# Performance work log

Hardware: AMD Instinct MI355X
Metric: run time of the kernel (lower is better)

## Reference

```python
import jax, jax.numpy as jnp
import numpy as np
from jax import lax

B_SZ = 64
D_MODEL = 768
D_INNER = 1536   # expand * d_model
D_STATE = 16
D_CONV = 4
DT_RANK = 48     # ceil(768/16)
ROWS, COLS = 16, 16
L = ROWS * COLS
LN_EPS = 1e-5


def setup_inputs() -> dict:
    key = jax.random.key(0)
    ks = jax.random.split(key, 16)
    def nrm(k, shape, s):
        return jax.random.normal(k, shape, jnp.float32) * s
    # A_log init as in Mamba: log(arange(1..d_state)) tiled over d_inner
    A_log = jnp.log(jnp.tile(jnp.arange(1, D_STATE + 1, dtype=jnp.float32)[None, :], (D_INNER, 1)))
    # dt bias init: inverse-softplus of dt ~ LogUniform(1e-3, 1e-1)
    def dt_bias_init(k):
        u = jax.random.uniform(k, (D_INNER,), jnp.float32)
        dt = jnp.exp(u * (np.log(0.1) - np.log(0.001)) + np.log(0.001))
        return dt + jnp.log(-jnp.expm1(-dt))
    dt_std = DT_RANK ** -0.5
    return {
        "hidden_states": jax.random.normal(ks[0], (B_SZ, L, D_MODEL), jnp.float32),
        "in_proj_w": nrm(ks[1], (2 * D_INNER, D_MODEL), 0.02),
        "conv_w": nrm(ks[2], (D_INNER, D_CONV), 0.2),
        "conv_bias": nrm(ks[3], (D_INNER,), 0.1),
        "conv_w_b": nrm(ks[4], (D_INNER, D_CONV), 0.2),
        "conv_bias_b": nrm(ks[5], (D_INNER,), 0.1),
        "x_proj_w": nrm(ks[6], (DT_RANK + 2 * D_STATE, D_INNER), 0.02),
        "x_proj_w_b": nrm(ks[7], (DT_RANK + 2 * D_STATE, D_INNER), 0.02),
        "dt_proj_w": jax.random.uniform(ks[8], (D_INNER, DT_RANK), jnp.float32, -dt_std, dt_std),
        "dt_proj_w_b": jax.random.uniform(ks[9], (D_INNER, DT_RANK), jnp.float32, -dt_std, dt_std),
        "dt_bias": dt_bias_init(ks[10]),
        "dt_bias_b": dt_bias_init(ks[11]),
        "A_log": A_log,
        "A_b_log": A_log,
        "Dp": jnp.ones((D_INNER,), jnp.float32),
        "Dp_b": jnp.ones((D_INNER,), jnp.float32),
        "ln_gamma": jnp.ones((D_INNER,), jnp.float32),
        "ln_beta": jnp.zeros((D_INNER,), jnp.float32),
        "out_proj_w": nrm(ks[12], (D_MODEL, D_INNER), 0.02),
    }


def _causal_conv_silu(x, w, b):
    # x: (B, D, L); depthwise causal conv (left-pad K-1) + SiLU
    y = lax.conv_general_dilated(x, w[:, None, :], (1,), [(D_CONV - 1, 0)],
                                 dimension_numbers=("NCH", "OIH", "NCH"),
                                 feature_group_count=D_INNER)
    return jax.nn.silu(y + b[None, :, None])


def _selective_scan(u, dt, A_log, Bm, Cm, dt_bias):
    # u, dt: (B, D, Lr); Bm, Cm: (B, N, Lr)
    A = -jnp.exp(A_log)                                     # (D, N)
    delta = jax.nn.softplus(dt + dt_bias[None, :, None])    # (B, D, Lr)
    dA = jnp.exp(jnp.einsum("bdl,dn->lbdn", delta, A))     # (Lr, B, D, N)
    dBu = jnp.einsum("bdl,bnl,bdl->lbdn", delta, Bm, u)    # (Lr, B, D, N)
    C_l = jnp.moveaxis(Cm, -1, 0)                           # (Lr, B, N)
    def step(h, inp):
        dA_t, dBu_t, C_t = inp
        h = dA_t * h + dBu_t
        return h, jnp.einsum("bdn,bn->bd", h, C_t)
    h0 = jnp.zeros(dA.shape[1:], dA.dtype)
    _, ys = lax.scan(step, h0, (dA, dBu, C_l))
    return jnp.moveaxis(ys, 0, -1)                          # (B, D, Lr)


def _direction(x, conv_w, conv_bias, x_proj_w, dt_proj_w, dt_bias, A_log, Dp):
    xc = _causal_conv_silu(x, conv_w, conv_bias)            # (B, D, L)
    x_comp = xc.reshape(-1, D_INNER, ROWS, COLS).mean(axis=3)  # (B, D, ROWS)
    x_dbl = jnp.einsum("bdl,ed->ble", x_comp, x_proj_w)    # (B, ROWS, R+2N)
    dt, Bm, Cm = jnp.split(x_dbl, [DT_RANK, DT_RANK + D_STATE], axis=-1)
    dt = jnp.einsum("blr,dr->bdl", dt, dt_proj_w)          # (B, D, ROWS)
    Bm = jnp.moveaxis(Bm, 1, 2)                             # (B, N, ROWS)
    Cm = jnp.moveaxis(Cm, 1, 2)
    y = _selective_scan(x_comp, dt, A_log, Bm, Cm, dt_bias)
    return jnp.repeat(y, COLS, axis=2) + Dp[None, :, None] * xc  # (B, D, L)


def reference(hidden_states, in_proj_w, conv_w, conv_bias, conv_w_b, conv_bias_b,
              x_proj_w, x_proj_w_b, dt_proj_w, dt_proj_w_b, dt_bias, dt_bias_b,
              A_log, A_b_log, Dp, Dp_b, ln_gamma, ln_beta, out_proj_w):
    xz = jnp.einsum("bld,ed->bel", hidden_states, in_proj_w)  # (B, 2*Di, L)
    x, z = jnp.split(xz, 2, axis=1)
    out_f = _direction(x, conv_w, conv_bias, x_proj_w, dt_proj_w, dt_bias, A_log, Dp)
    out_b = _direction(x[:, :, ::-1], conv_w_b, conv_bias_b, x_proj_w_b, dt_proj_w_b, dt_bias_b, A_b_log, Dp_b)
    comb = jnp.moveaxis((out_f + out_b[:, :, ::-1]) * 0.5, 1, 2)  # (B, L, Di)
    mu = comb.mean(-1, keepdims=True)
    var = comb.var(-1, keepdims=True)
    normed = (comb - mu) * lax.rsqrt(var + LN_EPS) * ln_gamma + ln_beta
    gated = normed * jax.nn.silu(jnp.moveaxis(z, 1, 2))
    return jnp.einsum("bld,od->blo", gated, out_proj_w)       # (B, L, d_model)
```

## Files before the change

kernel.cpp:

```cpp
#include <hip/hip_runtime.h>
#include <cstdint>
#include <cstddef>

typedef __bf16 bf16_t;
typedef __attribute__((ext_vector_type(2))) __bf16 bf16x2;
typedef __attribute__((ext_vector_type(8))) __bf16 bf16x8;
typedef __attribute__((ext_vector_type(4))) float f32x4;
typedef __attribute__((ext_vector_type(2))) float f32x2;

#define NB     64
#define LSEQ   256
#define DM     768
#define DI     1536
#define NSTATE 16
#define NROWS  16
#define RANK   48

#define BF16_PROBE 0x3F803F80u

__device__ __forceinline__ float bf2f(bf16_t v) { return (float)v; }

__device__ __forceinline__ float ldp(const void* p, size_t i, bool isbf) {
  return isbf ? (float)((const bf16_t*)p)[i] : ((const float*)p)[i];
}

__device__ __forceinline__ float silu_f(float x) {
  const float e = __expf(-fabsf(x));
  return (x >= 0.f) ? (x / (1.f + e)) : (x * e / (1.f + e));
}

__device__ __forceinline__ void async16(const bf16_t* g, bf16_t* l) {
  __builtin_amdgcn_global_load_lds(
      (const __attribute__((address_space(1))) void*)g,
      (__attribute__((address_space(3))) void*)l, 16, 0, 0);
}

__device__ __forceinline__ void cvt8(const void* in, bf16_t* out, int i, bool isbf) {
  if (isbf) {
    ((bf16x8*)out)[i] = ((const bf16x8*)in)[i];
  } else {
    const float* f = (const float*)in + (size_t)i * 8;
    f32x4 lo = *(const f32x4*)f, hi = *(const f32x4*)(f + 4);
    ((bf16x8*)out)[i] = (bf16x8){(bf16_t)lo.x, (bf16_t)lo.y, (bf16_t)lo.z, (bf16_t)lo.w,
                                 (bf16_t)hi.x, (bf16_t)hi.y, (bf16_t)hi.z, (bf16_t)hi.w};
  }
}

#define PREP_NH    6144
#define PREP_NWIN  1152
#define PREP_NWOUT 576
__global__ __launch_bounds__(256) void prep_kernel(
    const void* __restrict__ H, const void* __restrict__ Win,
    const void* __restrict__ Wout,
    bf16_t* __restrict__ Hb, bf16_t* __restrict__ Winb, bf16_t* __restrict__ Woutb,
    const uint32_t* __restrict__ probe)
{
  const bool isbf = (probe[0] == BF16_PROBE);
  int blk = blockIdx.x;
  if (blk < PREP_NH) {
    cvt8(H, Hb, blk * 256 + threadIdx.x, isbf);
  } else if (blk < PREP_NH + PREP_NWIN) {
    cvt8(Win, Winb, (blk - PREP_NH) * 256 + threadIdx.x, isbf);
  } else {
    cvt8(Wout, Woutb, (blk - PREP_NH - PREP_NWIN) * 256 + threadIdx.x, isbf);
  }
}

#define LDS_IDX(ab, db, half) (((ab) << 2) + ((db) << 1) + (half))

#define STAGE(ab, db, half, kt) do {                                          \
    const int _kt = ((kt) < NT) ? (kt) : (NT - 1);                            \
    const bf16_t* _g = (ab) ? B : A;                                          \
    const size_t _rb = ((ab) ? bn : bm) + (size_t)((half) * 128);             \
    bf16_t* _l = &sm[LDS_IDX(ab, db, half)][0];                               \
    _Pragma("unroll")                                                         \
    for (int _j = 0; _j < 2; _j++) {                                          \
      const int _c = wave * 2 + _j;                                           \
      async16(_g + (_rb + _c * 8 + srow) * (size_t)K + (size_t)_kt * 64 + scol,\
              _l + _c * 512);                                                 \
    }                                                                         \
  } while (0)

#define LOAD_A(db, mg) do {                                                   \
    _Pragma("unroll")                                                         \
    for (int _t = 0; _t < 2; _t++) {                                          \
      const int _mt = (mg) * 2 + _t;                                          \
      const int _lr = _mt * 32 + wm * 16 + r;                                 \
      const bf16_t* _b = &sm[LDS_IDX(0, db, _mt >> 2)][(_lr & 127) * 64];     \
      _Pragma("unroll")                                                       \
      for (int _s = 0; _s < 2; _s++)                                          \
        af[_t][_s] = *(const bf16x8*)&_b[(((_s * 4 + quad) ^ r7) * 8)];       \
    }                                                                         \
  } while (0)

#define LOAD_B(db) do {                                                       \
    _Pragma("unroll")                                                         \
    for (int _nt = 0; _nt < 4; _nt++) {                                       \
      const int _lr = _nt * 64 + wn * 16 + r;                                 \
      const bf16_t* _b = &sm[LDS_IDX(1, db, _lr >> 7)][(_lr & 127) * 64];     \
      _Pragma("unroll")                                                       \
      for (int _s = 0; _s < 2; _s++)                                          \
        bfr[_nt][_s] = *(const bf16x8*)&_b[(((_s * 4 + quad) ^ r7) * 8)];     \
    }                                                                         \
  } while (0)

#define MFMA16(mg) do {                                                       \
    __builtin_amdgcn_s_setprio(1);                                            \
    _Pragma("unroll")                                                         \
    for (int _t = 0; _t < 2; _t++)                                            \
    _Pragma("unroll")                                                         \
    for (int _nt = 0; _nt < 4; _nt++)                                         \
    _Pragma("unroll")                                                         \
    for (int _s = 0; _s < 2; _s++)                                            \
      acc[(mg) * 2 + _t][_nt] = __builtin_amdgcn_mfma_f32_16x16x32_bf16(      \
          af[_t][_s], bfr[_nt][_s], acc[(mg) * 2 + _t][_nt], 0, 0, 0);        \
    __builtin_amdgcn_s_setprio(0);                                            \
  } while (0)

#define BAR()    __builtin_amdgcn_s_barrier()
#define WAITL0() asm volatile("s_waitcnt lgkmcnt(0)" ::: "memory")
#define WAITV6() asm volatile("s_waitcnt vmcnt(6)" ::: "memory")

__global__ __launch_bounds__(512, 2) void gemm256_kernel(
    const bf16_t* __restrict__ A, const bf16_t* __restrict__ B,
    void* __restrict__ C, int M, int N, int K, int mode,
    bf16_t* __restrict__ xb)
{
  __shared__ bf16_t sm[8][8192];
  const int tid  = threadIdx.x;
  const int wave = tid >> 6, lane = tid & 63;
  const int wm = wave >> 2, wn = wave & 3;
  const int r = lane & 15, quad = lane >> 4, r7 = lane & 7;
  const int srow = lane >> 3;
  const int scol = ((lane & 7) ^ srow) * 8;
  const int NT = K >> 6;

  const int nwg  = gridDim.x * gridDim.y;
  const int orig = blockIdx.y * gridDim.x + blockIdx.x;
  const int swz  = (orig & 7) * (nwg >> 3) + (orig >> 3);
  const size_t bm = (size_t)(swz / gridDim.x) * 256;
  const size_t bn = (size_t)(swz % gridDim.x) * 256;

  f32x4 acc[8][4];
#pragma unroll
  for (int i = 0; i < 8; i++)
#pragma unroll
    for (int j = 0; j < 4; j++) acc[i][j] = (f32x4){0.f, 0.f, 0.f, 0.f};

  bf16x8 af[2][2];
  bf16x8 bfr[4][2];

  STAGE(1, 0, 0, 0);  STAGE(1, 0, 1, 0);  STAGE(0, 0, 0, 0);  STAGE(0, 0, 1, 0);
  asm volatile("s_waitcnt vmcnt(4)" ::: "memory");
  STAGE(1, 1, 0, 1);  STAGE(1, 1, 1, 1);  STAGE(0, 1, 0, 1);
  WAITV6();
  BAR();

  const int NP = NT >> 1;
  for (int i = 0; i < NP; ++i) {
    const int t1 = 2 * i + 1, t2 = 2 * i + 2, t3 = 2 * i + 3;
    LOAD_B(0); LOAD_A(0, 0); STAGE(0, 1, 1, t1);
    BAR(); WAITL0(); MFMA16(0); BAR();

    LOAD_A(0, 1); STAGE(1, 0, 0, t2);
    BAR(); WAITL0(); MFMA16(1); BAR();

    LOAD_A(0, 2); STAGE(1, 0, 1, t2);
    BAR(); WAITL0(); MFMA16(2); BAR();

    LOAD_A(0, 3); STAGE(0, 0, 0, t2);
    WAITV6();
    BAR(); WAITL0(); MFMA16(3); BAR();

    LOAD_B(1); LOAD_A(1, 0); STAGE(0, 0, 1, t2);
    BAR(); WAITL0(); MFMA16(0); BAR();

    LOAD_A(1, 1); STAGE(1, 1, 0, t3);
    BAR(); WAITL0(); MFMA16(1); BAR();

    LOAD_A(1, 2); STAGE(1, 1, 1, t3);
    BAR(); WAITL0(); MFMA16(2); BAR();

    LOAD_A(1, 3); STAGE(0, 1, 0, t3);
    WAITV6();
    BAR(); WAITL0(); MFMA16(3); BAR();
  }

  const int col16 = lane & 15;
  const int rb4 = quad * 4;

  if (mode == 0) {
#pragma unroll
    for (int mt = 0; mt < 8; mt++)
#pragma unroll
      for (int nt = 0; nt < 4; nt++)
#pragma unroll
        for (int v = 0; v < 4; v++) {
          const size_t m = bm + mt * 32 + wm * 16 + rb4 + v;
          const size_t n = bn + nt * 64 + wn * 16 + col16;
          ((float*)C)[m * (size_t)N + n] = acc[mt][nt][v];
        }
  } else {
    bf16_t* dst = (bn < (size_t)DI) ? xb : (bf16_t*)C;
    const size_t cb0 = (bn < (size_t)DI) ? bn : bn - DI;
#pragma unroll
    for (int mt = 0; mt < 8; mt++)
#pragma unroll
      for (int nt = 0; nt < 4; nt++)
#pragma unroll
        for (int v = 0; v < 4; v++) {
          const size_t m = bm + mt * 32 + wm * 16 + rb4 + v;
          dst[m * DI + cb0 + nt * 64 + wn * 16 + col16] = (bf16_t)acc[mt][nt][v];
        }
  }
}

__global__ __launch_bounds__(256) void conv_kernel(
    const bf16_t* __restrict__ xb,
    const void* __restrict__ cw_f, const void* __restrict__ cb_f,
    const void* __restrict__ cw_b, const void* __restrict__ cb_b,
    bf16_t* __restrict__ xc_f, bf16_t* __restrict__ xc_b,
    float* __restrict__ comp_f, float* __restrict__ comp_b,
    const uint32_t* __restrict__ probe)
{
  const bool isbf = (probe[0] == BF16_PROBE);
  int bi = blockIdx.x;
  const int chunk = bi & 3;
  bi >>= 2;
  const int b = bi / 3;
  const int pblk = bi % 3;
  const int d0 = (pblk * 256 + threadIdx.x) * 2;
  const int lr0 = chunk * 64;

  const float wf0a = ldp(cw_f, (size_t)d0 * 4 + 0, isbf),
              wf1a = ldp(cw_f, (size_t)d0 * 4 + 1, isbf),
              wf2a = ldp(cw_f, (size_t)d0 * 4 + 2, isbf),
              wf3a = ldp(cw_f, (size_t)d0 * 4 + 3, isbf);
  const float wf0c = ldp(cw_f, (size_t)(d0 + 1) * 4 + 0, isbf),
              wf1c = ldp(cw_f, (size_t)(d0 + 1) * 4 + 1, isbf),
              wf2c = ldp(cw_f, (size_t)(d0 + 1) * 4 + 2, isbf),
              wf3c = ldp(cw_f, (size_t)(d0 + 1) * 4 + 3, isbf);
  const float wb0a = ldp(cw_b, (size_t)d0 * 4 + 0, isbf),
              wb1a = ldp(cw_b, (size_t)d0 * 4 + 1, isbf),
              wb2a = ldp(cw_b, (size_t)d0 * 4 + 2, isbf),
              wb3a = ldp(cw_b, (size_t)d0 * 4 + 3, isbf);
  const float wb0c = ldp(cw_b, (size_t)(d0 + 1) * 4 + 0, isbf),
              wb1c = ldp(cw_b, (size_t)(d0 + 1) * 4 + 1, isbf),
              wb2c = ldp(cw_b, (size_t)(d0 + 1) * 4 + 2, isbf),
              wb3c = ldp(cw_b, (size_t)(d0 + 1) * 4 + 3, isbf);
  const float bfa = ldp(cb_f, d0, isbf), bfc = ldp(cb_f, d0 + 1, isbf);
  const float bba = ldp(cb_b, d0, isbf), bbc = ldp(cb_b, d0 + 1, isbf);

  const bf16_t* xrow = xb + (size_t)b * LSEQ * DI + d0;

  float t0a = 0.f, t1a = 0.f, t2a = 0.f, t3a = 0.f;
  float t0c = 0.f, t1c = 0.f, t2c = 0.f, t3c = 0.f;
  if (lr0 > 0) {
    bf16x2 v;
    v = *(const bf16x2*)&xrow[(size_t)(lr0 - 3) * DI]; t1a = (float)v.x; t1c = (float)v.y;
    v = *(const bf16x2*)&xrow[(size_t)(lr0 - 2) * DI]; t2a = (float)v.x; t2c = (float)v.y;
    v = *(const bf16x2*)&xrow[(size_t)(lr0 - 1) * DI]; t3a = (float)v.x; t3c = (float)v.y;
  }

  float sfa = 0.f, sfc = 0.f;
  float sba = 0.f, sbc = 0.f;
  for (int l = lr0; l < lr0 + 67; ++l) {
    float xa = 0.f, xcv = 0.f;
    if (l < LSEQ) {
      bf16x2 v = *(const bf16x2*)&xrow[(size_t)l * DI];
      xa = (float)v.x; xcv = (float)v.y;
    }
    t0a = t1a; t1a = t2a; t2a = t3a; t3a = xa;
    t0c = t1c; t1c = t2c; t2c = t3c; t3c = xcv;

    if (l < lr0 + 64) {
      const float ya = silu_f(bfa + wf0a * t0a + wf1a * t1a + wf2a * t2a + wf3a * t3a);
      const float yc = silu_f(bfc + wf0c * t0c + wf1c * t1c + wf2c * t2c + wf3c * t3c);
      *(bf16x2*)&xc_f[((size_t)b * LSEQ + l) * DI + d0] = (bf16x2){(bf16_t)ya, (bf16_t)yc};
      sfa += ya; sfc += yc;
      if ((l & 15) == 15) {
        *(f32x2*)&comp_f[((size_t)b * NROWS + (l >> 4)) * DI + d0] =
            (f32x2){sfa * (1.f / 16.f), sfc * (1.f / 16.f)};
        sfa = 0.f; sfc = 0.f;
      }
    }
    if (l >= lr0 + 3) {
      const int j = 258 - l;
      const float ya = silu_f(bba + wb0a * t3a + wb1a * t2a + wb2a * t1a + wb3a * t0a);
      const float yc = silu_f(bbc + wb0c * t3c + wb1c * t2c + wb2c * t1c + wb3c * t0c);
      *(bf16x2*)&xc_b[((size_t)b * LSEQ + j) * DI + d0] = (bf16x2){(bf16_t)ya, (bf16_t)yc};
      sba += ya; sbc += yc;
      if ((j & 15) == 0) {
        *(f32x2*)&comp_b[((size_t)b * NROWS + (j >> 4)) * DI + d0] =
            (f32x2){sba * (1.f / 16.f), sbc * (1.f / 16.f)};
        sba = 0.f; sbc = 0.f;
      }
    }
  }
}

__global__ __launch_bounds__(256) void xproj_kernel(
    const float* __restrict__ comp_f, const float* __restrict__ comp_b,
    const void* __restrict__ w_f, const void* __restrict__ w_b,
    float* __restrict__ xd_f, float* __restrict__ xd_b,
    const uint32_t* __restrict__ probe)
{
  const bool isbf = (probe[0] == BF16_PROBE);
  const int dir = blockIdx.y;
  const int rg = blockIdx.x;
  const float* comp = dir ? comp_b : comp_f;
  const void* W = dir ? w_b : w_f;
  float* out = dir ? xd_b : xd_f;
  const int r0 = rg * 8;

  __shared__ float xs[8][DI];
  for (int i = threadIdx.x; i < 8 * DI; i += 256)
    xs[i / DI][i % DI] = comp[(size_t)r0 * DI + i];
  __syncthreads();

  const int wave = threadIdx.x >> 6, lane = threadIdx.x & 63;
  for (int oo = 0; oo < 20; ++oo) {
    const int o = wave * 20 + oo;
    float a[8];
#pragma unroll
    for (int rr = 0; rr < 8; rr++) a[rr] = 0.f;
#pragma unroll
    for (int j = 0; j < 24; ++j) {
      const int k = lane + 64 * j;
      const float wv = ldp(W, (size_t)o * DI + k, isbf);
#pragma unroll
      for (int rr = 0; rr < 8; rr++) a[rr] += xs[rr][k] * wv;
    }
    for (int off = 32; off; off >>= 1) {
#pragma unroll
      for (int rr = 0; rr < 8; rr++) a[rr] += __shfl_down(a[rr], off);
    }
    if (lane == 0) {
#pragma unroll
      for (int rr = 0; rr < 8; rr++) out[(size_t)(r0 + rr) * 80 + o] = a[rr];
    }
  }
}

__global__ __launch_bounds__(256) void scan_kernel(
    const float* __restrict__ xd_fg, const float* __restrict__ xd_bg,
    const float* comp_f, const float* comp_b,
    const void* __restrict__ dtw_f, const void* __restrict__ dtw_b,
    const void* __restrict__ dtb_f, const void* __restrict__ dtb_b,
    const void* __restrict__ Al_f, const void* __restrict__ Al_b,
    float* y_fg, float* y_bg,
    const uint32_t* __restrict__ probe)
{
  const bool isbf = (probe[0] == BF16_PROBE);
  const int dir = blockIdx.y;
  const int b = blockIdx.x / 6;
  const int d = (blockIdx.x % 6) * 256 + threadIdx.x;
  const float* xd_g = dir ? xd_bg : xd_fg;
  const float* comp = dir ? comp_b : comp_f;
  const void* dtw = dir ? dtw_b : dtw_f;
  const void* dtb = dir ? dtb_b : dtb_f;
  const void* Al  = dir ? Al_b : Al_f;
  float* y = dir ? y_bg : y_fg;

  __shared__ float xd[NROWS * 80];
  for (int i = threadIdx.x; i < NROWS * 80; i += 256) xd[i] = xd_g[(size_t)b * (NROWS * 80) + i];
  __syncthreads();

  float dt[NROWS];
#pragma unroll
  for (int l = 0; l < NROWS; l++) dt[l] = 0.f;
  for (int r = 0; r < RANK; r++) {
    const float w = ldp(dtw, (size_t)d * RANK + r, isbf);
#pragma unroll
    for (int l = 0; l < NROWS; l++) dt[l] += xd[l * 80 + r] * w;
  }

  float A[NSTATE];
#pragma unroll
  for (int n = 0; n < NSTATE; n++) A[n] = -__expf(ldp(Al, (size_t)d * NSTATE + n, isbf));
  const float bias = ldp(dtb, d, isbf);

  float h[NSTATE];
#pragma unroll
  for (int n = 0; n < NSTATE; n++) h[n] = 0.f;

  for (int l = 0; l < NROWS; l++) {
    const float u = comp[((size_t)b * NROWS + l) * DI + d];
    const float dv = dt[l] + bias;
    const float delta = (dv > 15.f) ? dv : log1pf(__expf(dv));
    const float du = delta * u;
    float yv = 0.f;
#pragma unroll
    for (int n = 0; n < NSTATE; n++) {
      const float hn = __expf(delta * A[n]) * h[n] + du * xd[l * 80 + RANK + n];
      h[n] = hn;
      yv += hn * xd[l * 80 + RANK + NSTATE + n];
    }
    y[((size_t)b * NROWS + l) * DI + d] = yv;
  }
}

__global__ __launch_bounds__(256) void combine_kernel(
    const float* __restrict__ y_f, const float* __restrict__ y_b,
    bf16_t* xcg_f,
    const bf16_t* __restrict__ xc_b,
    const bf16_t* __restrict__ zb,
    const void* __restrict__ Dp, const void* __restrict__ Dp_b,
    const void* __restrict__ gamma, const void* __restrict__ beta,
    const uint32_t* __restrict__ probe)
{
  const bool isbf = (probe[0] == BF16_PROBE);
  const int m = blockIdx.x;
  const int b = m >> 8, l = m & 255;
  const int lr = LSEQ - 1 - l;
  const int tid = threadIdx.x;

  float v[6];
  float sum = 0.f, sq = 0.f;
#pragma unroll
  for (int i = 0; i < 6; i++) {
    const int d = tid + i * 256;
    const float cf = bf2f(xcg_f[((size_t)b * LSEQ + l) * DI + d]);
    const float cb = bf2f(xc_b[((size_t)b * LSEQ + lr) * DI + d]);
    const float vf = y_f[((size_t)b * NROWS + (l >> 4)) * DI + d] + ldp(Dp, d, isbf) * cf;
    const float vb = y_b[((size_t)b * NROWS + (lr >> 4)) * DI + d] + ldp(Dp_b, d, isbf) * cb;
    const float c = 0.5f * (vf + vb);
    v[i] = c; sum += c; sq += c * c;
  }
  for (int off = 32; off; off >>= 1) {
    sum += __shfl_down(sum, off);
    sq  += __shfl_down(sq, off);
  }
  __shared__ float rs[4], rq[4];
  if ((tid & 63) == 0) { rs[tid >> 6] = sum; rq[tid >> 6] = sq; }
  __syncthreads();
  const float S  = rs[0] + rs[1] + rs[2] + rs[3];
  const float SQ = rq[0] + rq[1] + rq[2] + rq[3];
  const float mu = S * (1.f / (float)DI);
  const float var = fmaxf(SQ * (1.f / (float)DI) - mu * mu, 0.f);
  const float rstd = rsqrtf(var + 1e-5f);
#pragma unroll
  for (int i = 0; i < 6; i++) {
    const int d = tid + i * 256;
    const float nrm = (v[i] - mu) * rstd * ldp(gamma, d, isbf) + ldp(beta, d, isbf);
    const float z = bf2f(zb[(size_t)m * DI + d]);
    xcg_f[(size_t)m * DI + d] = (bf16_t)(nrm * silu_f(z));
  }
}

extern "C" void kernel_launch(void* const* d_in, const int* in_sizes, int n_in,
                              void* d_out, int out_size, void* d_ws, size_t ws_size,
                              hipStream_t stream)
{
  (void)in_sizes; (void)n_in; (void)out_size; (void)ws_size;
  const void* H     = d_in[0];
  const void* Win   = d_in[1];
  const void* cw_f  = d_in[2];
  const void* cb_f  = d_in[3];
  const void* cw_b  = d_in[4];
  const void* cb_b  = d_in[5];
  const void* xpw_f = d_in[6];
  const void* xpw_b = d_in[7];
  const void* dtw_f = d_in[8];
  const void* dtw_b = d_in[9];
  const void* dtb_f = d_in[10];
  const void* dtb_b = d_in[11];
  const void* Al_f  = d_in[12];
  const void* Al_b  = d_in[13];
  const void* Dp    = d_in[14];
  const void* Dp_b  = d_in[15];
  const void* gam   = d_in[16];
  const void* bet   = d_in[17];
  const void* Wout  = d_in[18];
  const uint32_t* probe = (const uint32_t*)d_in[14];

  const size_t M = (size_t)NB * LSEQ;
  char* ws = (char*)d_ws;
  bf16_t* zb    = (bf16_t*)ws;  ws += M * DI * sizeof(bf16_t);
  bf16_t* xb    = (bf16_t*)ws;  ws += M * DI * sizeof(bf16_t);
  bf16_t* xc_f  = (bf16_t*)ws;  ws += M * DI * sizeof(bf16_t);
  bf16_t* xc_b  = (bf16_t*)ws;  ws += M * DI * sizeof(bf16_t);
  float* comp_f = (float*)ws;   ws += (size_t)NB * NROWS * DI * sizeof(float);
  float* comp_b = (float*)ws;   ws += (size_t)NB * NROWS * DI * sizeof(float);
  float* xd_f   = (float*)ws;   ws += (size_t)NB * NROWS * 80 * sizeof(float);
  float* xd_b   = (float*)ws;   ws += (size_t)NB * NROWS * 80 * sizeof(float);
  bf16_t* Hb    = (bf16_t*)ws;  ws += M * DM * sizeof(bf16_t);
  bf16_t* Winb  = (bf16_t*)ws;  ws += (size_t)(2 * DI) * DM * sizeof(bf16_t);
  bf16_t* Woutb = (bf16_t*)ws;  ws += (size_t)DM * DI * sizeof(bf16_t);

  prep_kernel<<<PREP_NH + PREP_NWIN + PREP_NWOUT, 256, 0, stream>>>(
      H, Win, Wout, Hb, Winb, Woutb, probe);

  gemm256_kernel<<<dim3(2 * DI / 256, M / 256), 512, 0, stream>>>(
      Hb, Winb, zb, (int)M, 2 * DI, DM, 1, xb);

  conv_kernel<<<dim3(768), 256, 0, stream>>>(
      xb, cw_f, cb_f, cw_b, cb_b, xc_f, xc_b, comp_f, comp_b, probe);

  xproj_kernel<<<dim3(128, 2), 256, 0, stream>>>(
      comp_f, comp_b, xpw_f, xpw_b, xd_f, xd_b, probe);

  scan_kernel<<<dim3(NB * (DI / 256), 2), 256, 0, stream>>>(
      xd_f, xd_b, comp_f, comp_b, dtw_f, dtw_b, dtb_f, dtb_b, Al_f, Al_b,
      comp_f, comp_b, probe);

  combine_kernel<<<dim3(NB * LSEQ), 256, 0, stream>>>(
      comp_f, comp_b, xc_f, xc_b, zb, Dp, Dp_b, gam, bet, probe);

  gemm256_kernel<<<dim3(DM / 256, M / 256), 512, 0, stream>>>(
      xc_f, Woutb, d_out, (int)M, DM, DI, 0, nullptr);
}
```

Baseline: 452.7 us.

## Recompute conv+SiLU in combine kernel instead of materializing xc_f/xc_b

The conv kernel no longer writes the full per-token conv outputs for both directions and only produces the pooled means. The combine kernel now reads a 7-row window of the raw x projection and recomputes the forward and backward causal conv plus SiLU on the fly. This removes two full M×DI bf16 writes and their later reads. In exchange it adds redundant window loads (mostly cache hits), per-element weight loads, and extra arithmetic in combine.

Result: slower. 806.8 us (+78.2%).

```diff
diff --git a/kernel.cpp b/kernel.cpp
--- a/kernel.cpp
+++ b/kernel.cpp
@@ -215,11 +215,10 @@
   }
 }
 
-__global__ __launch_bounds__(256) void conv_kernel(
+__global__ __launch_bounds__(256) void pool_kernel(
     const bf16_t* __restrict__ xb,
     const void* __restrict__ cw_f, const void* __restrict__ cb_f,
     const void* __restrict__ cw_b, const void* __restrict__ cb_b,
-    bf16_t* __restrict__ xc_f, bf16_t* __restrict__ xc_b,
     float* __restrict__ comp_f, float* __restrict__ comp_b,
     const uint32_t* __restrict__ probe)
 {
@@ -276,7 +275,6 @@
     if (l < lr0 + 64) {
       const float ya = silu_f(bfa + wf0a * t0a + wf1a * t1a + wf2a * t2a + wf3a * t3a);
       const float yc = silu_f(bfc + wf0c * t0c + wf1c * t1c + wf2c * t2c + wf3c * t3c);
-      *(bf16x2*)&xc_f[((size_t)b * LSEQ + l) * DI + d0] = (bf16x2){(bf16_t)ya, (bf16_t)yc};
       sfa += ya; sfc += yc;
       if ((l & 15) == 15) {
         *(f32x2*)&comp_f[((size_t)b * NROWS + (l >> 4)) * DI + d0] =
@@ -288,7 +286,6 @@
       const int j = 258 - l;
       const float ya = silu_f(bba + wb0a * t3a + wb1a * t2a + wb2a * t1a + wb3a * t0a);
       const float yc = silu_f(bbc + wb0c * t3c + wb1c * t2c + wb2c * t1c + wb3c * t0c);
-      *(bf16x2*)&xc_b[((size_t)b * LSEQ + j) * DI + d0] = (bf16x2){(bf16_t)ya, (bf16_t)yc};
       sba += ya; sbc += yc;
       if ((j & 15) == 0) {
         *(f32x2*)&comp_b[((size_t)b * NROWS + (j >> 4)) * DI + d0] =
@@ -402,9 +399,10 @@
 
 __global__ __launch_bounds__(256) void combine_kernel(
     const float* __restrict__ y_f, const float* __restrict__ y_b,
-    bf16_t* xcg_f,
-    const bf16_t* __restrict__ xc_b,
-    const bf16_t* __restrict__ zb,
+    const bf16_t* __restrict__ xb, const bf16_t* __restrict__ zb,
+    bf16_t* __restrict__ gated,
+    const void* __restrict__ cw_f, const void* __restrict__ cb_f,
+    const void* __restrict__ cw_b, const void* __restrict__ cb_b,
     const void* __restrict__ Dp, const void* __restrict__ Dp_b,
     const void* __restrict__ gamma, const void* __restrict__ beta,
     const uint32_t* __restrict__ probe)
@@ -412,18 +410,35 @@
   const bool isbf = (probe[0] == BF16_PROBE);
   const int m = blockIdx.x;
   const int b = m >> 8, l = m & 255;
-  const int lr = LSEQ - 1 - l;
   const int tid = threadIdx.x;
+
+  const bf16_t* xbase = xb + (size_t)b * LSEQ * DI;
+  const float* yfrow = y_f + ((size_t)b * NROWS + (l >> 4)) * DI;
+  const float* ybrow = y_b + ((size_t)b * NROWS + ((LSEQ - 1 - l) >> 4)) * DI;
 
   float v[6];
   float sum = 0.f, sq = 0.f;
 #pragma unroll
   for (int i = 0; i < 6; i++) {
     const int d = tid + i * 256;
-    const float cf = bf2f(xcg_f[((size_t)b * LSEQ + l) * DI + d]);
-    const float cb = bf2f(xc_b[((size_t)b * LSEQ + lr) * DI + d]);
-    const float vf = y_f[((size_t)b * NROWS + (l >> 4)) * DI + d] + ldp(Dp, d, isbf) * cf;
-    const float vb = y_b[((size_t)b * NROWS + (lr >> 4)) * DI + d] + ldp(Dp_b, d, isbf) * cb;
+    float W[7];
+#pragma unroll
+    for (int j = 0; j < 7; j++) {
+      const int rl = l - 3 + j;
+      W[j] = (rl >= 0 && rl < LSEQ) ? bf2f(xbase[(size_t)rl * DI + d]) : 0.f;
+    }
+    const float accf = ldp(cb_f, d, isbf)
+        + ldp(cw_f, (size_t)d * 4 + 0, isbf) * W[0]
+        + ldp(cw_f, (size_t)d * 4 + 1, isbf) * W[1]
+        + ldp(cw_f, (size_t)d * 4 + 2, isbf) * W[2]
+        + ldp(cw_f, (size_t)d * 4 + 3, isbf) * W[3];
+    const float accb = ldp(cb_b, d, isbf)
+        + ldp(cw_b, (size_t)d * 4 + 0, isbf) * W[6]
+        + ldp(cw_b, (size_t)d * 4 + 1, isbf) * W[5]
+        + ldp(cw_b, (size_t)d * 4 + 2, isbf) * W[4]
+        + ldp(cw_b, (size_t)d * 4 + 3, isbf) * W[3];
+    const float vf = yfrow[d] + ldp(Dp, d, isbf) * silu_f(accf);
+    const float vb = ybrow[d] + ldp(Dp_b, d, isbf) * silu_f(accb);
     const float c = 0.5f * (vf + vb);
     v[i] = c; sum += c; sq += c * c;
   }
@@ -444,7 +459,7 @@
     const int d = tid + i * 256;
     const float nrm = (v[i] - mu) * rstd * ldp(gamma, d, isbf) + ldp(beta, d, isbf);
     const float z = bf2f(zb[(size_t)m * DI + d]);
-    xcg_f[(size_t)m * DI + d] = (bf16_t)(nrm * silu_f(z));
+    gated[(size_t)m * DI + d] = (bf16_t)(nrm * silu_f(z));
   }
 }
 
@@ -478,8 +493,7 @@
   char* ws = (char*)d_ws;
   bf16_t* zb    = (bf16_t*)ws;  ws += M * DI * sizeof(bf16_t);
   bf16_t* xb    = (bf16_t*)ws;  ws += M * DI * sizeof(bf16_t);
-  bf16_t* xc_f  = (bf16_t*)ws;  ws += M * DI * sizeof(bf16_t);
-  bf16_t* xc_b  = (bf16_t*)ws;  ws += M * DI * sizeof(bf16_t);
+  bf16_t* gated = (bf16_t*)ws;  ws += M * DI * sizeof(bf16_t);
   float* comp_f = (float*)ws;   ws += (size_t)NB * NROWS * DI * sizeof(float);
   float* comp_b = (float*)ws;   ws += (size_t)NB * NROWS * DI * sizeof(float);
   float* xd_f   = (float*)ws;   ws += (size_t)NB * NROWS * 80 * sizeof(float);
@@ -494,8 +508,8 @@
   gemm256_kernel<<<dim3(2 * DI / 256, M / 256), 512, 0, stream>>>(
       Hb, Winb, zb, (int)M, 2 * DI, DM, 1, xb);
 
-  conv_kernel<<<dim3(768), 256, 0, stream>>>(
-      xb, cw_f, cb_f, cw_b, cb_b, xc_f, xc_b, comp_f, comp_b, probe);
+  pool_kernel<<<dim3(768), 256, 0, stream>>>(
+      xb, cw_f, cb_f, cw_b, cb_b, comp_f, comp_b, probe);
 
   xproj_kernel<<<dim3(128, 2), 256, 0, stream>>>(
       comp_f, comp_b, xpw_f, xpw_b, xd_f, xd_b, probe);
@@ -505,8 +519,9 @@
       comp_f, comp_b, probe);
 
   combine_kernel<<<dim3(NB * LSEQ), 256, 0, stream>>>(
-      comp_f, comp_b, xc_f, xc_b, zb, Dp, Dp_b, gam, bet, probe);
+      comp_f, comp_b, xb, zb, gated,
+      cw_f, cb_f, cw_b, cb_b, Dp, Dp_b, gam, bet, probe);
 
   gemm256_kernel<<<dim3(DM / 256, M / 256), 512, 0, stream>>>(
-      xc_f, Woutb, d_out, (int)M, DM, DI, 0, nullptr);
-}
+      gated, Woutb, d_out, (int)M, DM, DI, 0, nullptr);
+}
```

## Pre-convert small params to fp32 buffer and vectorize conv/combine kernels

Applied to the files above, without the earlier changes.

The prep kernel now also copies the conv weights, biases, Dp, LayerNorm gamma/beta and dt bias into one fp32 parameter buffer, and stores dt_proj weights transposed. This removes per-element dtype branching and gives coalesced weight reads in the scan. The conv and combine kernels are reworked to process 4 channels per thread with bf16x4/f32x4 vector loads and 384-thread blocks, and conv uses 32-row chunks over 512 blocks. The extra prep blocks add a small amount of work, and conv now has more halo overhead per chunk.

New measurement: 452.9 us. No clear change (+0.1%).

```diff
diff --git a/kernel.cpp b/kernel.cpp
--- a/kernel.cpp
+++ b/kernel.cpp
@@ -4,6 +4,7 @@
 
 typedef __bf16 bf16_t;
 typedef __attribute__((ext_vector_type(2))) __bf16 bf16x2;
+typedef __attribute__((ext_vector_type(4))) __bf16 bf16x4;
 typedef __attribute__((ext_vector_type(8))) __bf16 bf16x8;
 typedef __attribute__((ext_vector_type(4))) float f32x4;
 typedef __attribute__((ext_vector_type(2))) float f32x2;
@@ -46,13 +47,35 @@
   }
 }
 
+#define P_CWF   0
+#define P_CWB   6144
+#define P_CBF   12288
+#define P_CBB   13824
+#define P_DP    15360
+#define P_DPB   16896
+#define P_GAM   18432
+#define P_BET   19968
+#define P_DTBF  21504
+#define P_DTBB  23040
+#define P_DTWTF 24576
+#define P_DTWTB 98304
+#define P_TOTAL 172032
+
 #define PREP_NH    6144
 #define PREP_NWIN  1152
 #define PREP_NWOUT 576
+#define PREP_NPAR  672
 __global__ __launch_bounds__(256) void prep_kernel(
     const void* __restrict__ H, const void* __restrict__ Win,
     const void* __restrict__ Wout,
+    const void* __restrict__ cw_f, const void* __restrict__ cw_b,
+    const void* __restrict__ cb_f, const void* __restrict__ cb_b,
+    const void* __restrict__ Dp, const void* __restrict__ Dp_b,
+    const void* __restrict__ gam, const void* __restrict__ bet,
+    const void* __restrict__ dtb_f, const void* __restrict__ dtb_b,
+    const void* __restrict__ dtw_f, const void* __restrict__ dtw_b,
     bf16_t* __restrict__ Hb, bf16_t* __restrict__ Winb, bf16_t* __restrict__ Woutb,
+    float* __restrict__ P,
     const uint32_t* __restrict__ probe)
 {
   const bool isbf = (probe[0] == BF16_PROBE);
@@ -61,8 +84,29 @@
     cvt8(H, Hb, blk * 256 + threadIdx.x, isbf);
   } else if (blk < PREP_NH + PREP_NWIN) {
     cvt8(Win, Winb, (blk - PREP_NH) * 256 + threadIdx.x, isbf);
+  } else if (blk < PREP_NH + PREP_NWIN + PREP_NWOUT) {
+    cvt8(Wout, Woutb, (blk - PREP_NH - PREP_NWIN) * 256 + threadIdx.x, isbf);
   } else {
-    cvt8(Wout, Woutb, (blk - PREP_NH - PREP_NWIN) * 256 + threadIdx.x, isbf);
+    const int p = (blk - PREP_NH - PREP_NWIN - PREP_NWOUT) * 256 + (int)threadIdx.x;
+    float v;
+    if (p < P_CWB)            v = ldp(cw_f, p, isbf);
+    else if (p < P_CBF)       v = ldp(cw_b, p - P_CWB, isbf);
+    else if (p < P_CBB)       v = ldp(cb_f, p - P_CBF, isbf);
+    else if (p < P_DP)        v = ldp(cb_b, p - P_CBB, isbf);
+    else if (p < P_DPB)       v = ldp(Dp,   p - P_DP, isbf);
+    else if (p < P_GAM)       v = ldp(Dp_b, p - P_DPB, isbf);
+    else if (p < P_BET)       v = ldp(gam,  p - P_GAM, isbf);
+    else if (p < P_DTBF)      v = ldp(bet,  p - P_BET, isbf);
+    else if (p < P_DTBB)      v = ldp(dtb_f, p - P_DTBF, isbf);
+    else if (p < P_DTWTF)     v = ldp(dtb_b, p - P_DTBB, isbf);
+    else if (p < P_DTWTB) {
+      const int q = p - P_DTWTF, r = q / DI, d = q - r * DI;
+      v = ldp(dtw_f, (size_t)d * RANK + r, isbf);
+    } else {
+      const int q = p - P_DTWTB, r = q / DI, d = q - r * DI;
+      v = ldp(dtw_b, (size_t)d * RANK + r, isbf);
+    }
+    P[p] = v;
   }
 }
 
@@ -215,85 +259,86 @@
   }
 }
 
-__global__ __launch_bounds__(256) void conv_kernel(
-    const bf16_t* __restrict__ xb,
-    const void* __restrict__ cw_f, const void* __restrict__ cb_f,
-    const void* __restrict__ cw_b, const void* __restrict__ cb_b,
+__global__ __launch_bounds__(384) void conv_kernel(
+    const bf16_t* __restrict__ xb, const float* __restrict__ P,
     bf16_t* __restrict__ xc_f, bf16_t* __restrict__ xc_b,
-    float* __restrict__ comp_f, float* __restrict__ comp_b,
-    const uint32_t* __restrict__ probe)
-{
-  const bool isbf = (probe[0] == BF16_PROBE);
-  int bi = blockIdx.x;
-  const int chunk = bi & 3;
-  bi >>= 2;
-  const int b = bi / 3;
-  const int pblk = bi % 3;
-  const int d0 = (pblk * 256 + threadIdx.x) * 2;
-  const int lr0 = chunk * 64;
-
-  const float wf0a = ldp(cw_f, (size_t)d0 * 4 + 0, isbf),
-              wf1a = ldp(cw_f, (size_t)d0 * 4 + 1, isbf),
-              wf2a = ldp(cw_f, (size_t)d0 * 4 + 2, isbf),
-              wf3a = ldp(cw_f, (size_t)d0 * 4 + 3, isbf);
-  const float wf0c = ldp(cw_f, (size_t)(d0 + 1) * 4 + 0, isbf),
-              wf1c = ldp(cw_f, (size_t)(d0 + 1) * 4 + 1, isbf),
-              wf2c = ldp(cw_f, (size_t)(d0 + 1) * 4 + 2, isbf),
-              wf3c = ldp(cw_f, (size_t)(d0 + 1) * 4 + 3, isbf);
-  const float wb0a = ldp(cw_b, (size_t)d0 * 4 + 0, isbf),
-              wb1a = ldp(cw_b, (size_t)d0 * 4 + 1, isbf),
-              wb2a = ldp(cw_b, (size_t)d0 * 4 + 2, isbf),
-              wb3a = ldp(cw_b, (size_t)d0 * 4 + 3, isbf);
-  const float wb0c = ldp(cw_b, (size_t)(d0 + 1) * 4 + 0, isbf),
-              wb1c = ldp(cw_b, (size_t)(d0 + 1) * 4 + 1, isbf),
-              wb2c = ldp(cw_b, (size_t)(d0 + 1) * 4 + 2, isbf),
-              wb3c = ldp(cw_b, (size_t)(d0 + 1) * 4 + 3, isbf);
-  const float bfa = ldp(cb_f, d0, isbf), bfc = ldp(cb_f, d0 + 1, isbf);
-  const float bba = ldp(cb_b, d0, isbf), bbc = ldp(cb_b, d0 + 1, isbf);
+    float* __restrict__ comp_f, float* __restrict__ comp_b)
+{
+  const int bi = blockIdx.x;
+  const int chunk = bi & 7;
+  const int b = bi >> 3;
+  const int d0 = (int)threadIdx.x * 4;
+  const int lr0 = chunk * 32;
+
+  f32x4 wf[4], wb_[4];
+#pragma unroll
+  for (int c = 0; c < 4; c++) {
+    wf[c]  = *(const f32x4*)&P[P_CWF + (d0 + c) * 4];
+    wb_[c] = *(const f32x4*)&P[P_CWB + (d0 + c) * 4];
+  }
+  const f32x4 cbf = *(const f32x4*)&P[P_CBF + d0];
+  const f32x4 cbb = *(const f32x4*)&P[P_CBB + d0];
 
   const bf16_t* xrow = xb + (size_t)b * LSEQ * DI + d0;
 
-  float t0a = 0.f, t1a = 0.f, t2a = 0.f, t3a = 0.f;
-  float t0c = 0.f, t1c = 0.f, t2c = 0.f, t3c = 0.f;
+  float t0[4], t1[4], t2[4], t3[4];
+#pragma unroll
+  for (int c = 0; c < 4; c++) { t0[c] = t1[c] = t2[c] = t3[c] = 0.f; }
   if (lr0 > 0) {
-    bf16x2 v;
-    v = *(const bf16x2*)&xrow[(size_t)(lr0 - 3) * DI]; t1a = (float)v.x; t1c = (float)v.y;
-    v = *(const bf16x2*)&xrow[(size_t)(lr0 - 2) * DI]; t2a = (float)v.x; t2c = (float)v.y;
-    v = *(const bf16x2*)&xrow[(size_t)(lr0 - 1) * DI]; t3a = (float)v.x; t3c = (float)v.y;
-  }
-
-  float sfa = 0.f, sfc = 0.f;
-  float sba = 0.f, sbc = 0.f;
-  for (int l = lr0; l < lr0 + 67; ++l) {
-    float xa = 0.f, xcv = 0.f;
+    const bf16x4 h1 = *(const bf16x4*)&xrow[(size_t)(lr0 - 3) * DI];
+    const bf16x4 h2 = *(const bf16x4*)&xrow[(size_t)(lr0 - 2) * DI];
+    const bf16x4 h3 = *(const bf16x4*)&xrow[(size_t)(lr0 - 1) * DI];
+#pragma unroll
+    for (int c = 0; c < 4; c++) { t1[c] = (float)h1[c]; t2[c] = (float)h2[c]; t3[c] = (float)h3[c]; }
+  }
+
+  float sf[4] = {0.f, 0.f, 0.f, 0.f};
+  float sb[4] = {0.f, 0.f, 0.f, 0.f};
+  for (int l = lr0; l < lr0 + 35; ++l) {
+    float xv[4] = {0.f, 0.f, 0.f, 0.f};
     if (l < LSEQ) {
-      bf16x2 v = *(const bf16x2*)&xrow[(size_t)l * DI];
-      xa = (float)v.x; xcv = (float)v.y;
-    }
-    t0a = t1a; t1a = t2a; t2a = t3a; t3a = xa;
-    t0c = t1c; t1c = t2c; t2c = t3c; t3c = xcv;
-
-    if (l < lr0 + 64) {
-      const float ya = silu_f(bfa + wf0a * t0a + wf1a * t1a + wf2a * t2a + wf3a * t3a);
-      const float yc = silu_f(bfc + wf0c * t0c + wf1c * t1c + wf2c * t2c + wf3c * t3c);
-      *(bf16x2*)&xc_f[((size_t)b * LSEQ + l) * DI + d0] = (bf16x2){(bf16_t)ya, (bf16_t)yc};
-      sfa += ya; sfc += yc;
+      const bf16x4 v = *(const bf16x4*)&xrow[(size_t)l * DI];
+#pragma unroll
+      for (int c = 0; c < 4; c++) xv[c] = (float)v[c];
+    }
+#pragma unroll
+    for (int c = 0; c < 4; c++) { t0[c] = t1[c]; t1[c] = t2[c]; t2[c] = t3[c]; t3[c] = xv[c]; }
+
+    if (l < lr0 + 32) {
+      bf16x4 yo;
+      float y[4];
+#pragma unroll
+      for (int c = 0; c < 4; c++) {
+        y[c] = silu_f(cbf[c] + wf[c].x * t0[c] + wf[c].y * t1[c] + wf[c].z * t2[c] + wf[c].w * t3[c]);
+        yo[c] = (bf16_t)y[c];
+        sf[c] += y[c];
+      }
+      *(bf16x4*)&xc_f[((size_t)b * LSEQ + l) * DI + d0] = yo;
       if ((l & 15) == 15) {
-        *(f32x2*)&comp_f[((size_t)b * NROWS + (l >> 4)) * DI + d0] =
-            (f32x2){sfa * (1.f / 16.f), sfc * (1.f / 16.f)};
-        sfa = 0.f; sfc = 0.f;
+        *(f32x4*)&comp_f[((size_t)b * NROWS + (l >> 4)) * DI + d0] =
+            (f32x4){sf[0] * (1.f / 16.f), sf[1] * (1.f / 16.f),
+                    sf[2] * (1.f / 16.f), sf[3] * (1.f / 16.f)};
+#pragma unroll
+        for (int c = 0; c < 4; c++) sf[c] = 0.f;
       }
     }
     if (l >= lr0 + 3) {
       const int j = 258 - l;
-      const float ya = silu_f(bba + wb0a * t3a + wb1a * t2a + wb2a * t1a + wb3a * t0a);
-      const float yc = silu_f(bbc + wb0c * t3c + wb1c * t2c + wb2c * t1c + wb3c * t0c);
-      *(bf16x2*)&xc_b[((size_t)b * LSEQ + j) * DI + d0] = (bf16x2){(bf16_t)ya, (bf16_t)yc};
-      sba += ya; sbc += yc;
+      bf16x4 yo;
+      float y[4];
+#pragma unroll
+      for (int c = 0; c < 4; c++) {
+        y[c] = silu_f(cbb[c] + wb_[c].x * t3[c] + wb_[c].y * t2[c] + wb_[c].z * t1[c] + wb_[c].w * t0[c]);
+        yo[c] = (bf16_t)y[c];
+        sb[c] += y[c];
+      }
+      *(bf16x4*)&xc_b[((size_t)b * LSEQ + j) * DI + d0] = yo;
       if ((j & 15) == 0) {
-        *(f32x2*)&comp_b[((size_t)b * NROWS + (j >> 4)) * DI + d0] =
-            (f32x2){sba * (1.f / 16.f), sbc * (1.f / 16.f)};
-        sba = 0.f; sbc = 0.f;
+        *(f32x4*)&comp_b[((size_t)b * NROWS + (j >> 4)) * DI + d0] =
+            (f32x4){sb[0] * (1.f / 16.f), sb[1] * (1.f / 16.f),
+                    sb[2] * (1.f / 16.f), sb[3] * (1.f / 16.f)};
+#pragma unroll
+        for (int c = 0; c < 4; c++) sb[c] = 0.f;
       }
     }
   }
@@ -345,8 +390,7 @@
 __global__ __launch_bounds__(256) void scan_kernel(
     const float* __restrict__ xd_fg, const float* __restrict__ xd_bg,
     const float* comp_f, const float* comp_b,
-    const void* __restrict__ dtw_f, const void* __restrict__ dtw_b,
-    const void* __restrict__ dtb_f, const void* __restrict__ dtb_b,
+    const float* __restrict__ P,
     const void* __restrict__ Al_f, const void* __restrict__ Al_b,
     float* y_fg, float* y_bg,
     const uint32_t* __restrict__ probe)
@@ -357,8 +401,8 @@
   const int d = (blockIdx.x % 6) * 256 + threadIdx.x;
   const float* xd_g = dir ? xd_bg : xd_fg;
   const float* comp = dir ? comp_b : comp_f;
-  const void* dtw = dir ? dtw_b : dtw_f;
-  const void* dtb = dir ? dtb_b : dtb_f;
+  const float* dtwT = P + (dir ? P_DTWTB : P_DTWTF);
+  const float bias = P[(dir ? P_DTBB : P_DTBF) + d];
   const void* Al  = dir ? Al_b : Al_f;
   float* y = dir ? y_bg : y_fg;
 
@@ -370,7 +414,7 @@
 #pragma unroll
   for (int l = 0; l < NROWS; l++) dt[l] = 0.f;
   for (int r = 0; r < RANK; r++) {
-    const float w = ldp(dtw, (size_t)d * RANK + r, isbf);
+    const float w = dtwT[(size_t)r * DI + d];
 #pragma unroll
     for (int l = 0; l < NROWS; l++) dt[l] += xd[l * 80 + r] * w;
   }
@@ -378,7 +422,6 @@
   float A[NSTATE];
 #pragma unroll
   for (int n = 0; n < NSTATE; n++) A[n] = -__expf(ldp(Al, (size_t)d * NSTATE + n, isbf));
-  const float bias = ldp(dtb, d, isbf);
 
   float h[NSTATE];
 #pragma unroll
@@ -400,52 +443,59 @@
   }
 }
 
-__global__ __launch_bounds__(256) void combine_kernel(
+__global__ __launch_bounds__(384) void combine_kernel(
     const float* __restrict__ y_f, const float* __restrict__ y_b,
     bf16_t* xcg_f,
     const bf16_t* __restrict__ xc_b,
     const bf16_t* __restrict__ zb,
-    const void* __restrict__ Dp, const void* __restrict__ Dp_b,
-    const void* __restrict__ gamma, const void* __restrict__ beta,
-    const uint32_t* __restrict__ probe)
-{
-  const bool isbf = (probe[0] == BF16_PROBE);
+    const float* __restrict__ P)
+{
   const int m = blockIdx.x;
   const int b = m >> 8, l = m & 255;
   const int lr = LSEQ - 1 - l;
   const int tid = threadIdx.x;
-
-  float v[6];
+  const int wave = tid >> 6, lane = tid & 63;
+  const int d0 = tid * 4;
+
+  const bf16x4 cfv = *(const bf16x4*)&xcg_f[((size_t)b * LSEQ + l) * DI + d0];
+  const bf16x4 cbv = *(const bf16x4*)&xc_b[((size_t)b * LSEQ + lr) * DI + d0];
+  const f32x4 yfv = *(const f32x4*)&y_f[((size_t)b * NROWS + (l >> 4)) * DI + d0];
+  const f32x4 ybv = *(const f32x4*)&y_b[((size_t)b * NROWS + (lr >> 4)) * DI + d0];
+  const f32x4 dp  = *(const f32x4*)&P[P_DP + d0];
+  const f32x4 dpb = *(const f32x4*)&P[P_DPB + d0];
+
+  float v[4];
   float sum = 0.f, sq = 0.f;
 #pragma unroll
-  for (int i = 0; i < 6; i++) {
-    const int d = tid + i * 256;
-    const float cf = bf2f(xcg_f[((size_t)b * LSEQ + l) * DI + d]);
-    const float cb = bf2f(xc_b[((size_t)b * LSEQ + lr) * DI + d]);
-    const float vf = y_f[((size_t)b * NROWS + (l >> 4)) * DI + d] + ldp(Dp, d, isbf) * cf;
-    const float vb = y_b[((size_t)b * NROWS + (lr >> 4)) * DI + d] + ldp(Dp_b, d, isbf) * cb;
-    const float c = 0.5f * (vf + vb);
-    v[i] = c; sum += c; sq += c * c;
+  for (int c = 0; c < 4; c++) {
+    const float cc = 0.5f * ((yfv[c] + dp[c] * (float)cfv[c]) +
+                             (ybv[c] + dpb[c] * (float)cbv[c]));
+    v[c] = cc; sum += cc; sq += cc * cc;
   }
   for (int off = 32; off; off >>= 1) {
     sum += __shfl_down(sum, off);
     sq  += __shfl_down(sq, off);
   }
-  __shared__ float rs[4], rq[4];
-  if ((tid & 63) == 0) { rs[tid >> 6] = sum; rq[tid >> 6] = sq; }
+  __shared__ float rs[6], rq[6];
+  if (lane == 0) { rs[wave] = sum; rq[wave] = sq; }
   __syncthreads();
-  const float S  = rs[0] + rs[1] + rs[2] + rs[3];
-  const float SQ = rq[0] + rq[1] + rq[2] + rq[3];
+  float S = 0.f, SQ = 0.f;
+#pragma unroll
+  for (int w = 0; w < 6; w++) { S += rs[w]; SQ += rq[w]; }
   const float mu = S * (1.f / (float)DI);
   const float var = fmaxf(SQ * (1.f / (float)DI) - mu * mu, 0.f);
   const float rstd = rsqrtf(var + 1e-5f);
-#pragma unroll
-  for (int i = 0; i < 6; i++) {
-    const int d = tid + i * 256;
-    const float nrm = (v[i] - mu) * rstd * ldp(gamma, d, isbf) + ldp(beta, d, isbf);
-    const float z = bf2f(zb[(size_t)m * DI + d]);
-    xcg_f[(size_t)m * DI + d] = (bf16_t)(nrm * silu_f(z));
-  }
+
+  const f32x4 gm = *(const f32x4*)&P[P_GAM + d0];
+  const f32x4 bt = *(const f32x4*)&P[P_BET + d0];
+  const bf16x4 zv = *(const bf16x4*)&zb[(size_t)m * DI + d0];
+  bf16x4 outv;
+#pragma unroll
+  for (int c = 0; c < 4; c++) {
+    const float nrm = (v[c] - mu) * rstd * gm[c] + bt[c];
+    outv[c] = (bf16_t)(nrm * silu_f((float)zv[c]));
+  }
+  *(bf16x4*)&xcg_f[(size_t)m * DI + d0] = outv;
 }
 
 extern "C" void kernel_launch(void* const* d_in, const int* in_sizes, int n_in,
@@ -487,25 +537,26 @@
   bf16_t* Hb    = (bf16_t*)ws;  ws += M * DM * sizeof(bf16_t);
   bf16_t* Winb  = (bf16_t*)ws;  ws += (size_t)(2 * DI) * DM * sizeof(bf16_t);
   bf16_t* Woutb = (bf16_t*)ws;  ws += (size_t)DM * DI * sizeof(bf16_t);
-
-  prep_kernel<<<PREP_NH + PREP_NWIN + PREP_NWOUT, 256, 0, stream>>>(
-      H, Win, Wout, Hb, Winb, Woutb, probe);
+  float* P      = (float*)ws;   ws += (size_t)P_TOTAL * sizeof(float);
+
+  prep_kernel<<<PREP_NH + PREP_NWIN + PREP_NWOUT + PREP_NPAR, 256, 0, stream>>>(
+      H, Win, Wout, cw_f, cw_b, cb_f, cb_b, Dp, Dp_b, gam, bet,
+      dtb_f, dtb_b, dtw_f, dtw_b, Hb, Winb, Woutb, P, probe);
 
   gemm256_kernel<<<dim3(2 * DI / 256, M / 256), 512, 0, stream>>>(
       Hb, Winb, zb, (int)M, 2 * DI, DM, 1, xb);
 
-  conv_kernel<<<dim3(768), 256, 0, stream>>>(
-      xb, cw_f, cb_f, cw_b, cb_b, xc_f, xc_b, comp_f, comp_b, probe);
+  conv_kernel<<<dim3(512), 384, 0, stream>>>(
+      xb, P, xc_f, xc_b, comp_f, comp_b);
 
   xproj_kernel<<<dim3(128, 2), 256, 0, stream>>>(
       comp_f, comp_b, xpw_f, xpw_b, xd_f, xd_b, probe);
 
   scan_kernel<<<dim3(NB * (DI / 256), 2), 256, 0, stream>>>(
-      xd_f, xd_b, comp_f, comp_b, dtw_f, dtw_b, dtb_f, dtb_b, Al_f, Al_b,
-      comp_f, comp_b, probe);
-
-  combine_kernel<<<dim3(NB * LSEQ), 256, 0, stream>>>(
-      comp_f, comp_b, xc_f, xc_b, zb, Dp, Dp_b, gam, bet, probe);
+      xd_f, xd_b, comp_f, comp_b, P, Al_f, Al_b, comp_f, comp_b, probe);
+
+  combine_kernel<<<dim3(NB * LSEQ), 384, 0, stream>>>(
+      comp_f, comp_b, xc_f, xc_b, zb, P);
 
   gemm256_kernel<<<dim3(DM / 256, M / 256), 512, 0, stream>>>(
       xc_f, Woutb, d_out, (int)M, DM, DI, 0, nullptr);
```
